# Performance work log

Hardware: AMD Instinct MI355X
Metric: run time of the kernel (lower is better)

The kernel has to match this reference:

```python
import jax, jax.numpy as jnp
import numpy as np

B = 64      # num graphs
NPG = 800   # nodes per graph
N = B * NPG
EPG = 6400  # edges per graph (avg degree 8)
APG = 64    # feasible actions per graph
H = 4       # attention heads
C = 64      # hidden channels per head
OUT = 128   # out_channels


def _gat_params(key, fin, h, c, concat):
    k1, k2, k3 = jax.random.split(key, 3)
    s = 1.0 / np.sqrt(fin)
    W = jax.random.uniform(k1, (fin, h * c), jnp.float32, -s, s)
    a_src = jax.random.uniform(k2, (h, c), jnp.float32, -s, s)
    a_dst = jax.random.uniform(k3, (h, c), jnp.float32, -s, s)
    b = jnp.zeros((h * c if concat else c,), jnp.float32)
    return W, a_src, a_dst, b


def _lin_params(key, fin, fout):
    k1, k2 = jax.random.split(key)
    s = 1.0 / np.sqrt(fin)
    W = jax.random.uniform(k1, (fin, fout), jnp.float32, -s, s)
    b = jax.random.uniform(k2, (fout,), jnp.float32, -s, s)
    return W, b


def setup_inputs() -> dict:
    key = jax.random.key(0)
    ks = list(jax.random.split(key, 24))
    x = jax.random.normal(ks[0], (N, 5), jnp.float32)
    offs = jnp.arange(B, dtype=jnp.int32) * NPG
    src = jax.random.randint(ks[1], (B, EPG), 0, NPG, jnp.int32) + offs[:, None]
    dst = jax.random.randint(ks[2], (B, EPG), 0, NPG, jnp.int32) + offs[:, None]
    edge_index = jnp.stack([src.reshape(-1), dst.reshape(-1)])
    batch = jnp.repeat(jnp.arange(B, dtype=jnp.int32), NPG)
    actions_idx = (jax.random.randint(ks[3], (B, APG, 2), 0, NPG, jnp.int32)
                   + offs[:, None, None]).reshape(-1, 2)
    tabu_label = (jax.random.uniform(ks[4], (B * APG, 1)) < 0.5).astype(jnp.float32)
    inp = dict(x=x, edge_index=edge_index, batch=batch,
               actions_idx=actions_idx, tabu_label=tabu_label)
    names = ['f1', 'f2', 'f3', 'b1', 'b2', 'b3']
    fins = [3, H * C, H * C, 3, H * C, H * C]
    hs = [H, H, 1, H, H, 1]
    cs = [C, C, OUT, C, C, OUT]
    concats = [True, True, False, True, True, False]
    for i, nm in enumerate(names):
        W, a_s, a_d, b = _gat_params(ks[5 + i], fins[i], hs[i], cs[i], concats[i])
        inp[nm + '_W'] = W; inp[nm + '_as'] = a_s; inp[nm + '_ad'] = a_d; inp[nm + '_b'] = b
    dims = [(8 * OUT + 1, 2 * OUT), (2 * OUT, 2 * OUT), (2 * OUT, 2 * OUT), (2 * OUT, 1)]
    for i, (fi, fo) in enumerate(dims):
        W, b = _lin_params(ks[12 + i], fi, fo)
        inp['p_W%d' % (i + 1)] = W; inp['p_b%d' % (i + 1)] = b
    return inp


def _gat(h, s, d, W, a_src, a_dst, bias, concat):
    # PyG GATConv: project, per-edge attention, softmax over target index, scatter-add
    n = h.shape[0]
    Hh, Cc = a_src.shape
    xp = (h @ W).reshape(n, Hh, Cc)                      # [N,H,C]
    al_s = (xp * a_src).sum(-1)                          # [N,H]
    al_d = (xp * a_dst).sum(-1)                          # [N,H]
    e = jax.nn.leaky_relu(al_s[s] + al_d[d], 0.2)        # [E,H]
    m = jax.ops.segment_max(e, d, num_segments=n)
    ex = jnp.exp(e - m[d])
    den = jax.ops.segment_sum(ex, d, num_segments=n)
    alpha = ex / (den[d] + 1e-16)
    out = jax.ops.segment_sum(xp[s] * alpha[..., None], d, num_segments=n)  # [N,H,C]
    out = out.reshape(n, Hh * Cc) if concat else out.mean(axis=1)
    return out + bias


def reference(x, edge_index, batch, actions_idx, tabu_label,
              f1_W, f1_as, f1_ad, f1_b, f2_W, f2_as, f2_ad, f2_b,
              f3_W, f3_as, f3_ad, f3_b, b1_W, b1_as, b1_ad, b1_b,
              b2_W, b2_as, b2_ad, b2_b, b3_W, b3_as, b3_ad, b3_b,
              p_W1, p_b1, p_W2, p_b2, p_W3, p_b3, p_W4, p_b4):
    n = x.shape[0]
    ar = jnp.arange(n, dtype=edge_index.dtype)
    ei = jnp.concatenate([edge_index, jnp.stack([ar, ar])], axis=1)  # add_self_loops
    src, dst = ei[0], ei[1]
    # forward branch (flow source_to_target)
    hf = x[:, jnp.array([0, 1, 3])]
    hf = jax.nn.elu(_gat(hf, src, dst, f1_W, f1_as, f1_ad, f1_b, True))
    hf = jax.nn.elu(_gat(hf, src, dst, f2_W, f2_as, f2_ad, f2_b, True))
    hf3 = _gat(hf, src, dst, f3_W, f3_as, f3_ad, f3_b, False)
    # backward branch (flow target_to_source == reversed edges)
    hb = x[:, jnp.array([0, 2, 4])]
    hb = jax.nn.elu(_gat(hb, dst, src, b1_W, b1_as, b1_ad, b1_b, True))
    hb = jax.nn.elu(_gat(hb, dst, src, b2_W, b2_as, b2_ad, b2_b, True))
    hb3 = _gat(hb, dst, src, b3_W, b3_as, b3_ad, b3_b, False)
    h_node = jnp.concatenate([hf3, hb3], axis=-1)        # [N, 2*OUT]
    counts = jax.ops.segment_sum(jnp.ones((n,), x.dtype), batch, num_segments=B)
    g_pool = jax.ops.segment_sum(h_node, batch, num_segments=B) / counts[:, None]
    node_h = jnp.concatenate([h_node, g_pool[batch]], axis=-1)  # [N, 4*OUT]
    action_h = jnp.concatenate([node_h[actions_idx[:, 0]],
                                node_h[actions_idx[:, 1]],
                                tabu_label], axis=-1)    # [A, 8*OUT+1]
    h = jnp.tanh(action_h @ p_W1 + p_b1)
    h = jnp.tanh(h @ p_W2 + p_b2)
    h = jnp.tanh(h @ p_W3 + p_b3)
    score = (h @ p_W4 + p_b4).reshape(B, APG)
    log_prob = jax.nn.log_softmax(score, axis=-1)        # [B, APG]
    entropy = -(jnp.exp(log_prob) * log_prob).sum(-1, keepdims=True)  # [B,1]
    return (log_prob, entropy)
```

## Files before the change

kernel.cpp:

```cpp
#include <hip/hip_runtime.h>
#include <hip/hip_bf16.h>
#include <math.h>

constexpr int NN  = 51200;
constexpr int EE  = 409600;
constexpr int BB  = 64;
constexpr int APG = 64;
constexpr int NPG = 800;
constexpr int SCAN_N = 2 * NN;
constexpr int NA = BB * APG;
constexpr int KF = 1056;

typedef __bf16 bf16x8 __attribute__((ext_vector_type(8)));
typedef float f32x4 __attribute__((ext_vector_type(4)));
typedef float f32x2 __attribute__((ext_vector_type(2)));
typedef __attribute__((address_space(1))) const void g_void;
typedef __attribute__((address_space(3))) void l_void;

__device__ __forceinline__ float leaky(float x) { return x > 0.f ? x : 0.2f * x; }
__device__ __forceinline__ float bflo(unsigned w) { return __uint_as_float(w << 16); }
__device__ __forceinline__ float bfhi(unsigned w) { return __uint_as_float(w & 0xffff0000u); }
__device__ __forceinline__ unsigned short f2b(float x) {
  __hip_bfloat16 h = __float2bfloat16(x);
  unsigned short u;
  __builtin_memcpy(&u, &h, 2);
  return u;
}
__device__ __forceinline__ unsigned pack2(float a, float b) {
  return (unsigned)f2b(a) | ((unsigned)f2b(b) << 16);
}

__global__ void count_kernel(const int* __restrict__ ei, int* cnt) {
  int e = blockIdx.x * blockDim.x + threadIdx.x;
  if (e >= EE) return;
  int s = ei[e], d = ei[EE + e];
  atomicAdd(&cnt[d], 1);
  atomicAdd(&cnt[NN + s], 1);
}

__global__ __launch_bounds__(256) void scan1_kernel(const int* __restrict__ cnt,
                                                    int* __restrict__ rp,
                                                    int* __restrict__ bsum) {
  __shared__ int wsum[4];
  int b = blockIdx.x, t = threadIdx.x;
  int base = b * 1024 + t * 4;
  int4 v = *(const int4*)(cnt + base);
  int s = v.x + v.y + v.z + v.w;
  int lane = t & 63, wv = t >> 6;
  int incl = s;
  for (int off = 1; off < 64; off <<= 1) {
    int u = __shfl_up(incl, off);
    if (lane >= off) incl += u;
  }
  if (lane == 63) wsum[wv] = incl;
  __syncthreads();
  int woff = 0;
  for (int i = 0; i < wv; i++) woff += wsum[i];
  int excl = woff + incl - s;
  rp[base] = excl;
  rp[base + 1] = excl + v.x;
  rp[base + 2] = excl + v.x + v.y;
  rp[base + 3] = excl + v.x + v.y + v.z;
  if (t == 255) bsum[b] = woff + incl;
}

__global__ void scan2_kernel(const int* __restrict__ bsum, int* __restrict__ boff,
                             int* __restrict__ rp) {
  __shared__ int w0;
  int t = threadIdx.x;
  int v = (t < 100) ? bsum[t] : 0;
  int lane = t & 63;
  int incl = v;
  for (int off = 1; off < 64; off <<= 1) {
    int u = __shfl_up(incl, off);
    if (lane >= off) incl += u;
  }
  if (t == 63) w0 = incl;
  __syncthreads();
  int excl = incl - v + ((t >= 64) ? w0 : 0);
  if (t < 100) boff[t] = excl;
  if (t == 99) rp[SCAN_N] = excl + v;
}

__global__ __launch_bounds__(256) void scan3_kernel(int* __restrict__ rp,
                                                    const int* __restrict__ boff) {
  int b = blockIdx.x;
  int off = boff[b];
  int i = b * 1024 + threadIdx.x * 4;
  int4 v = *(int4*)(rp + i);
  v.x += off; v.y += off; v.z += off; v.w += off;
  *(int4*)(rp + i) = v;
}

__global__ void fill_kernel(const int* __restrict__ ei, const int* __restrict__ rp,
                            int* pos, int* __restrict__ col) {
  int e = blockIdx.x * blockDim.x + threadIdx.x;
  if (e >= EE) return;
  int s = ei[e], d = ei[EE + e];
  int p = atomicAdd(&pos[d], 1);
  col[rp[d] + p] = s;
  int q = atomicAdd(&pos[NN + s], 1);
  col[rp[NN + s] + q] = d;
}

__global__ __launch_bounds__(256) void precomp_kernel(const float* __restrict__ Wf,
                                                      const float* __restrict__ Wb,
                                                      const float* __restrict__ asf,
                                                      const float* __restrict__ adf,
                                                      const float* __restrict__ asb,
                                                      const float* __restrict__ adb,
                                                      float* __restrict__ wa) {
  int wave = (blockIdx.x * blockDim.x + threadIdx.x) >> 6;
  int lane = threadIdx.x & 63;
  if (wave >= 48) return;
  int dir = wave / 24, sd = (wave / 12) % 2, h = (wave / 3) % 4, c = wave % 3;
  const float* W = dir ? Wb : Wf;
  const float* a = dir ? (sd ? adb : asb) : (sd ? adf : asf);
  float v = W[c * 256 + h * 64 + lane] * a[h * 64 + lane];
  for (int off = 1; off < 64; off <<= 1) v += __shfl_xor(v, off);
  if (lane == 0) wa[wave] = v;
}

__global__ __launch_bounds__(256) void lin1_kernel(const float* __restrict__ x,
                                                   const float* __restrict__ Wf,
                                                   const float* __restrict__ Wb,
                                                   __hip_bfloat16* __restrict__ out) {
  int idx = blockIdx.x * 256 + threadIdx.x;
  int n = idx >> 5, grp = idx & 31;
  int dir = (n >= NN) ? 1 : 0;
  int node = dir ? n - NN : n;
  const float* W = dir ? Wb : Wf;
  int c1 = dir ? 2 : 1, c2 = dir ? 4 : 3;
  float f0 = x[node * 5], f1 = x[node * 5 + c1], f2 = x[node * 5 + c2];
  int j0 = grp * 8;
  float v[8];
#pragma unroll
  for (int j = 0; j < 8; j++)
    v[j] = f0 * W[j0 + j] + f1 * W[256 + j0 + j] + f2 * W[512 + j0 + j];
  uint4 u;
  u.x = pack2(v[0], v[1]);
  u.y = pack2(v[2], v[3]);
  u.z = pack2(v[4], v[5]);
  u.w = pack2(v[6], v[7]);
  *(uint4*)(out + (size_t)n * 256 + j0) = u;
}

__global__ __launch_bounds__(256) void al1_kernel(const float* __restrict__ x,
                                                  const float* __restrict__ wa,
                                                  float* __restrict__ al_s,
                                                  float* __restrict__ al_d) {
  int idx = blockIdx.x * 256 + threadIdx.x;
  int n = idx >> 2, h = idx & 3;
  int dir = (n >= NN) ? 1 : 0;
  int node = dir ? n - NN : n;
  int c1 = dir ? 2 : 1, c2 = dir ? 4 : 3;
  float f0 = x[node * 5], f1 = x[node * 5 + c1], f2 = x[node * 5 + c2];
  const float* ws = wa + dir * 24 + h * 3;
  const float* wd = wa + dir * 24 + 12 + h * 3;
  al_s[idx] = f0 * ws[0] + f1 * ws[1] + f2 * ws[2];
  al_d[idx] = f0 * wd[0] + f1 * wd[1] + f2 * wd[2];
}

template <int HH>
__global__ __launch_bounds__(256) void alpha_kernel(const float* __restrict__ als,
                                                    const float* __restrict__ ald,
                                                    const int* __restrict__ rp,
                                                    const int* __restrict__ col,
                                                    float* __restrict__ alpha,
                                                    float* __restrict__ alpha_self) {
  int b = blockIdx.x;
  int xcd = b & 7, q = b >> 3;
  int g2 = (q / 25) * 8 + xcd;
  int d = g2 * 800 + (q % 25) * 32 + (threadIdx.x >> 3);
  int slot = threadIdx.x & 7;
  int off_row = (d >= NN) ? NN : 0;
  float ald_loc[HH], self_lg[HH];
#pragma unroll
  for (int h = 0; h < HH; h++) {
    ald_loc[h] = ald[d * HH + h];
    self_lg[h] = leaky(als[d * HH + h] + ald_loc[h]);
  }
  int beg = rp[d], end = rp[d + 1];
  int i0 = beg + slot;
  bool have = i0 < end;
  int s0 = col[have ? i0 : beg] + off_row;
  float mx[HH], lg0[HH];
#pragma unroll
  for (int h = 0; h < HH; h++) mx[h] = self_lg[h];
  if (have) {
#pragma unroll
    for (int h = 0; h < HH; h++) {
      lg0[h] = leaky(als[s0 * HH + h] + ald_loc[h]);
      mx[h] = fmaxf(mx[h], lg0[h]);
    }
  }
  for (int i = i0 + 8; i < end; i += 8) {
    int s = col[i] + off_row;
#pragma unroll
    for (int h = 0; h < HH; h++) mx[h] = fmaxf(mx[h], leaky(als[s * HH + h] + ald_loc[h]));
  }
#pragma unroll
  for (int h = 0; h < HH; h++) {
    mx[h] = fmaxf(mx[h], __shfl_xor(mx[h], 1));
    mx[h] = fmaxf(mx[h], __shfl_xor(mx[h], 2));
    mx[h] = fmaxf(mx[h], __shfl_xor(mx[h], 4));
  }
  float sm[HH], w0[HH];
#pragma unroll
  for (int h = 0; h < HH; h++) sm[h] = 0.f;
  if (have) {
#pragma unroll
    for (int h = 0; h < HH; h++) {
      w0[h] = __expf(lg0[h] - mx[h]);
      sm[h] += w0[h];
    }
  }
  for (int i = i0 + 8; i < end; i += 8) {
    int s = col[i] + off_row;
#pragma unroll
    for (int h = 0; h < HH; h++) {
      float w = __expf(leaky(als[s * HH + h] + ald_loc[h]) - mx[h]);
      sm[h] += w;
      alpha[(size_t)i * HH + h] = w;
    }
  }
#pragma unroll
  for (int h = 0; h < HH; h++) {
    sm[h] += __shfl_xor(sm[h], 1);
    sm[h] += __shfl_xor(sm[h], 2);
    sm[h] += __shfl_xor(sm[h], 4);
  }
  float inv[HH];
#pragma unroll
  for (int h = 0; h < HH; h++)
    inv[h] = 1.f / (sm[h] + __expf(self_lg[h] - mx[h]) + 1e-16f);
  if (have) {
#pragma unroll
    for (int h = 0; h < HH; h++) alpha[(size_t)i0 * HH + h] = w0[h] * inv[h];
  }
  for (int i = i0 + 8; i < end; i += 8)
#pragma unroll
    for (int h = 0; h < HH; h++) alpha[(size_t)i * HH + h] *= inv[h];
  if (slot == 0) {
#pragma unroll
    for (int h = 0; h < HH; h++)
      alpha_self[d * HH + h] = __expf(self_lg[h] - mx[h]) * inv[h];
  }
}

template <int ND>
__device__ __forceinline__ void load_dw(const unsigned* p, unsigned* w) {
  if constexpr (ND == 4) {
    uint4 v = *(const uint4*)p;
    w[0] = v.x; w[1] = v.y; w[2] = v.z; w[3] = v.w;
  } else {
    uint2 v = *(const uint2*)p;
    w[0] = v.x; w[1] = v.y;
  }
}
__device__ __forceinline__ f32x2 unpk(unsigned w) {
  f32x2 v;
  v.x = bflo(w);
  v.y = bfhi(w);
  return v;
}

template <int HH, int CC, int OUT_SPLIT>
__global__ __launch_bounds__(256) void spmm_kernel(const __hip_bfloat16* __restrict__ xp,
                                                   const float* __restrict__ alpha,
                                                   const float* __restrict__ alpha_self,
                                                   const int* __restrict__ rp,
                                                   const int* __restrict__ col,
                                                   const float* __restrict__ biasf,
                                                   const float* __restrict__ biasb,
                                                   __hip_bfloat16* __restrict__ out_bf,
                                                   int do_elu) {
  constexpr int HC = HH * CC;
  constexpr int CPL = HC / 32;
  constexpr int NW = CPL / 2;
  int b = blockIdx.x;
  int xcd = b & 7, q = b >> 3;
  int g2 = (q / 200) * 8 + xcd;
  int d = g2 * 800 + (q % 200) * 4 + (threadIdx.x >> 6);
  int off_row = (d >= NN) ? NN : 0;
  const float* bias = (d >= NN) ? biasb : biasf;
  int lane = threadIdx.x & 63;
  int sub = lane & 31, g = lane >> 5;
  int h_l = (sub * CPL) / CC;
  const unsigned* xw = (const unsigned*)xp;
  size_t rowoff = (size_t)sub * NW;
  f32x2 acc[NW];
#pragma unroll
  for (int j = 0; j < NW; j++) acc[j] = (f32x2)(0.f);
  int beg = rp[d], end = rp[d + 1];
  int deg = end - beg;
  if (g == 0) {
    float a = alpha_self[d * HH + h_l];
    unsigned w[NW];
    load_dw<NW>(xw + (size_t)d * (HC / 2) + rowoff, w);
#pragma unroll
    for (int q2 = 0; q2 < NW; q2++) acc[q2] += a * unpk(w[q2]);
  }
  for (int it = 0; it * 4 < deg; it++) {
    int e1 = beg + it * 4 + g;
    int e2 = e1 + 2;
    bool p1 = e1 < end, p2 = e2 < end;
    int ec1 = p1 ? e1 : beg, ec2 = p2 ? e2 : beg;
    int s1 = col[ec1] + off_row, s2 = col[ec2] + off_row;
    float a1 = p1 ? alpha[(size_t)ec1 * HH + h_l] : 0.f;
    float a2 = p2 ? alpha[(size_t)ec2 * HH + h_l] : 0.f;
    unsigned w1[NW], w2[NW];
    load_dw<NW>(xw + (size_t)s1 * (HC / 2) + rowoff, w1);
    load_dw<NW>(xw + (size_t)s2 * (HC / 2) + rowoff, w2);
#pragma unroll
    for (int q2 = 0; q2 < NW; q2++)
      acc[q2] += a1 * unpk(w1[q2]) + a2 * unpk(w2[q2]);
  }
#pragma unroll
  for (int j = 0; j < NW; j++) {
    acc[j].x += __shfl_xor(acc[j].x, 32);
    acc[j].y += __shfl_xor(acc[j].y, 32);
  }
  if (g == 0) {
    float v[CPL];
#pragma unroll
    for (int j = 0; j < NW; j++) {
      v[2 * j] = acc[j].x + bias[sub * CPL + 2 * j];
      v[2 * j + 1] = acc[j].y + bias[sub * CPL + 2 * j + 1];
    }
    if (do_elu) {
#pragma unroll
      for (int j = 0; j < CPL; j++) v[j] = v[j] > 0.f ? v[j] : (__expf(v[j]) - 1.f);
    }
    unsigned* ob;
    if constexpr (OUT_SPLIT) {
      int nd = (d < NN) ? d : d - NN;
      int oo = (d < NN) ? 0 : 64;
      ob = (unsigned*)out_bf + (size_t)nd * 128 + oo + sub * NW;
    } else {
      ob = (unsigned*)out_bf + (size_t)d * (HC / 2) + rowoff;
    }
#pragma unroll
    for (int q2 = 0; q2 < NW; q2++)
      ob[q2] = pack2(v[2 * q2], v[2 * q2 + 1]);
  }
}

__global__ void castW2_kernel(const float* __restrict__ W0, const float* __restrict__ W1,
                              __hip_bfloat16* __restrict__ Wt0,
                              __hip_bfloat16* __restrict__ Wt1,
                              int K, int N, int Kp) {
  int idx = blockIdx.x * 256 + threadIdx.x;
  int tot = N * Kp;
  if (idx >= 2 * tot) return;
  const float* W = (idx < tot) ? W0 : W1;
  __hip_bfloat16* Wt = (idx < tot) ? Wt0 : Wt1;
  int i = (idx < tot) ? idx : idx - tot;
  int n = i / Kp, k = i % Kp;
  Wt[i] = (k < K) ? __float2bfloat16(W[(size_t)k * N + n]) : __float2bfloat16(0.f);
}

template <int EPI, int ALH, int ALCC>
__global__ __launch_bounds__(256) void gemm_mfma(const __hip_bfloat16* __restrict__ A,
                                                 const __hip_bfloat16* __restrict__ Bt0,
                                                 const __hip_bfloat16* __restrict__ Bt1,
                                                 __hip_bfloat16* __restrict__ Cb,
                                                 const float* __restrict__ bias0,
                                                 const float* __restrict__ bias1,
                                                 const float* __restrict__ asv0,
                                                 const float* __restrict__ asv1,
                                                 const float* __restrict__ adv0,
                                                 const float* __restrict__ adv1,
                                                 float* __restrict__ al_s,
                                                 float* __restrict__ al_d,
                                                 int M, int N, int K, int Mhalf) {
  __shared__ __align__(16) __hip_bfloat16 As[128 * 32];
  __shared__ __align__(16) __hip_bfloat16 Bs[128 * 32];
  int t = threadIdx.x;
  int wave = t >> 6, lane = t & 63;
  int wm = (wave >> 1) * 64, wn = (wave & 1) * 64;
  int bm = blockIdx.y * 128, bn = blockIdx.x * 128;
  bool second = bm >= Mhalf;
  const __hip_bfloat16* Bt = second ? Bt1 : Bt0;
  const float* bias = second ? bias1 : bias0;
  const float* asv = second ? asv1 : asv0;
  const float* adv = second ? adv1 : adv0;

  int r0 = t >> 2, c0 = (t & 3) * 8;
  const __hip_bfloat16* Ag0 = A + (size_t)(bm + r0) * K + c0;
  const __hip_bfloat16* Ag1 = A + (size_t)(bm + r0 + 64) * K + c0;
  const __hip_bfloat16* Bg0 = Bt + (size_t)(bn + r0) * K + c0;
  const __hip_bfloat16* Bg1 = Bt + (size_t)(bn + r0 + 64) * K + c0;
  __hip_bfloat16* Asp0 = As + t * 8;
  __hip_bfloat16* Asp1 = As + 64 * 8 * 4 + t * 8;
  __hip_bfloat16* Bsp0 = Bs + t * 8;
  __hip_bfloat16* Bsp1 = Bs + 64 * 8 * 4 + t * 8;

  f32x4 acc[4][4];
#pragma unroll
  for (int i = 0; i < 4; i++)
#pragma unroll
    for (int j = 0; j < 4; j++) acc[i][j] = (f32x4)(0.f);

  int frag_off = (lane & 15) * 32 + (lane >> 4) * 8;
  const __hip_bfloat16* Ab = As + wm * 32 + frag_off;
  const __hip_bfloat16* Bb = Bs + wn * 32 + frag_off;

  for (int k0 = 0; k0 < K; k0 += 32) {
    __syncthreads();
    __builtin_amdgcn_global_load_lds((g_void*)(Ag0 + k0), (l_void*)Asp0, 16, 0, 0);
    __builtin_amdgcn_global_load_lds((g_void*)(Ag1 + k0), (l_void*)Asp1, 16, 0, 0);
    __builtin_amdgcn_global_load_lds((g_void*)(Bg0 + k0), (l_void*)Bsp0, 16, 0, 0);
    __builtin_amdgcn_global_load_lds((g_void*)(Bg1 + k0), (l_void*)Bsp1, 16, 0, 0);
    __syncthreads();
    bf16x8 af[4], bfr[4];
#pragma unroll
    for (int i = 0; i < 4; i++) af[i] = *(const bf16x8*)(Ab + i * 16 * 32);
#pragma unroll
    for (int j = 0; j < 4; j++) bfr[j] = *(const bf16x8*)(Bb + j * 16 * 32);
#pragma unroll
    for (int i = 0; i < 4; i++)
#pragma unroll
      for (int j = 0; j < 4; j++)
        acc[i][j] = __builtin_amdgcn_mfma_f32_16x16x32_bf16(af[i], bfr[j], acc[i][j], 0, 0, 0);
  }

  int cr = (lane >> 4) * 4, cc = lane & 15;

  if constexpr (ALH > 0) {
    int head = (bn + wn) / ALCC;
    float as_c[4], ad_c[4];
#pragma unroll
    for (int j = 0; j < 4; j++) {
      int colx = bn + wn + j * 16 + cc;
      as_c[j] = asv[colx];
      ad_c[j] = adv[colx];
    }
#pragma unroll
    for (int i = 0; i < 4; i++)
#pragma unroll
      for (int r = 0; r < 4; r++) {
        float ps = 0.f, pd = 0.f;
#pragma unroll
        for (int j = 0; j < 4; j++) {
          ps += acc[i][j][r] * as_c[j];
          pd += acc[i][j][r] * ad_c[j];
        }
        ps += __shfl_xor(ps, 1); pd += __shfl_xor(pd, 1);
        ps += __shfl_xor(ps, 2); pd += __shfl_xor(pd, 2);
        ps += __shfl_xor(ps, 4); pd += __shfl_xor(pd, 4);
        ps += __shfl_xor(ps, 8); pd += __shfl_xor(pd, 8);
        if ((lane & 15) == 0) {
          int row = bm + wm + i * 16 + cr + r;
          if (ALCC > 64) {
            atomicAdd(&al_s[row * ALH + head], ps);
            atomicAdd(&al_d[row * ALH + head], pd);
          } else {
            al_s[row * ALH + head] = ps;
            al_d[row * ALH + head] = pd;
          }
        }
      }
  }

#pragma unroll
  for (int i = 0; i < 4; i++)
#pragma unroll
    for (int j = 0; j < 4; j++) {
      int colx = bn + wn + j * 16 + cc;
      float bs = (EPI == 2) ? bias[colx] : 0.f;
#pragma unroll
      for (int r = 0; r < 4; r++) {
        float v = acc[i][j][r];
        if (EPI == 2) v = tanhf(v + bs);
        Cb[(size_t)(bm + wm + i * 16 + cr + r) * N + colx] = __float2bfloat16(v);
      }
    }
}

__global__ void pool1_kernel(const __hip_bfloat16* __restrict__ h_node,
                             float* __restrict__ part) {
  int g = blockIdx.y, c = blockIdx.x, t = threadIdx.x;
  const unsigned* base = (const unsigned*)h_node + ((size_t)g * NPG + c * 100) * 128 + t;
  f32x2 s = (f32x2)(0.f);
  for (int i = 0; i < 100; i++) {
    unsigned w = base[(size_t)i * 128];
    s += unpk(w);
  }
  part[(size_t)(g * 8 + c) * 256 + 2 * t] = s.x;
  part[(size_t)(g * 8 + c) * 256 + 2 * t + 1] = s.y;
}

__global__ void pool2_kernel(const float* __restrict__ part, float* __restrict__ g_pool) {
  int g = blockIdx.x, t = threadIdx.x;
  float s = 0.f;
  for (int c = 0; c < 8; c++) s += part[(size_t)(g * 8 + c) * 256 + t];
  g_pool[g * 256 + t] = s * (1.f / NPG);
}

__global__ __launch_bounds__(256) void buildfeat_kernel(const __hip_bfloat16* __restrict__ h_node,
                                                        const float* __restrict__ g_pool,
                                                        const int* __restrict__ actions,
                                                        const float* __restrict__ tabu,
                                                        const int* __restrict__ batch,
                                                        __hip_bfloat16* __restrict__ feat) {
  int a = (blockIdx.x * blockDim.x + threadIdx.x) >> 6;
  int lane = threadIdx.x & 63;
  if (a >= NA) return;
  int n0 = actions[a * 2], n1 = actions[a * 2 + 1];
  int g = batch[n0];
  ushort4 v0 = *(const ushort4*)(h_node + (size_t)n0 * 256 + lane * 4);
  float4 vg = *(const float4*)(g_pool + (size_t)g * 256 + lane * 4);
  ushort4 v1 = *(const ushort4*)(h_node + (size_t)n1 * 256 + lane * 4);
  __hip_bfloat16* fr = feat + (size_t)a * KF;
  ushort4 ug = make_ushort4(f2b(vg.x), f2b(vg.y), f2b(vg.z), f2b(vg.w));
  *(ushort4*)(fr + lane * 4) = v0;
  *(ushort4*)(fr + 256 + lane * 4) = ug;
  *(ushort4*)(fr + 512 + lane * 4) = v1;
  *(ushort4*)(fr + 768 + lane * 4) = ug;
  if (lane < 8) {
    float t0 = (lane == 0) ? tabu[a] : 0.f;
    ushort4 u = make_ushort4(f2b(t0), 0, 0, 0);
    *(ushort4*)(fr + 1024 + lane * 4) = u;
  }
}

__global__ __launch_bounds__(256) void gemv_kernel(const __hip_bfloat16* __restrict__ y,
                                                   const float* __restrict__ W4,
                                                   const float* __restrict__ b4,
                                                   float* __restrict__ scores) {
  int a = (blockIdx.x * blockDim.x + threadIdx.x) >> 6;
  int lane = threadIdx.x & 63;
  if (a >= NA) return;
  const unsigned* row = (const unsigned*)(y + (size_t)a * 256);
  float s = 0.f;
#pragma unroll
  for (int q = 0; q < 2; q++) {
    unsigned w = row[lane * 2 + q];
    s += bflo(w) * W4[lane * 4 + 2 * q] + bfhi(w) * W4[lane * 4 + 2 * q + 1];
  }
  for (int off = 1; off < 64; off <<= 1) s += __shfl_xor(s, off);
  if (lane == 0) scores[a] = s + b4[0];
}

__global__ void softmax_kernel(const float* __restrict__ scores, float* __restrict__ out) {
  int g = (blockIdx.x * blockDim.x + threadIdx.x) >> 6;
  int lane = threadIdx.x & 63;
  if (g >= BB) return;
  float s = scores[g * 64 + lane];
  float m = s;
  for (int off = 1; off < 64; off <<= 1) m = fmaxf(m, __shfl_xor(m, off));
  float ex = expf(s - m);
  float sum = ex;
  for (int off = 1; off < 64; off <<= 1) sum += __shfl_xor(sum, off);
  float lp = s - m - logf(sum);
  out[g * 64 + lane] = lp;
  float pe = (ex / sum) * lp;
  for (int off = 1; off < 64; off <<= 1) pe += __shfl_xor(pe, off);
  if (lane == 0) out[BB * APG + g] = -pe;
}

extern "C" void kernel_launch(void* const* d_in, const int* in_sizes, int n_in,
                              void* d_out, int out_size, void* d_ws, size_t ws_size,
                              hipStream_t stream) {
  const float* x = (const float*)d_in[0];
  const int* ei = (const int*)d_in[1];
  const int* batch = (const int*)d_in[2];
  const int* actions = (const int*)d_in[3];
  const float* tabu = (const float*)d_in[4];
  const float* fW[3] = {(const float*)d_in[5], (const float*)d_in[9], (const float*)d_in[13]};
  const float* fas[3] = {(const float*)d_in[6], (const float*)d_in[10], (const float*)d_in[14]};
  const float* fad[3] = {(const float*)d_in[7], (const float*)d_in[11], (const float*)d_in[15]};
  const float* fb[3] = {(const float*)d_in[8], (const float*)d_in[12], (const float*)d_in[16]};
  const float* bW[3] = {(const float*)d_in[17], (const float*)d_in[21], (const float*)d_in[25]};
  const float* bas[3] = {(const float*)d_in[18], (const float*)d_in[22], (const float*)d_in[26]};
  const float* bad[3] = {(const float*)d_in[19], (const float*)d_in[23], (const float*)d_in[27]};
  const float* bb[3] = {(const float*)d_in[20], (const float*)d_in[24], (const float*)d_in[28]};
  const float* pW1 = (const float*)d_in[29];
  const float* pb1 = (const float*)d_in[30];
  const float* pW2 = (const float*)d_in[31];
  const float* pb2 = (const float*)d_in[32];
  const float* pW3 = (const float*)d_in[33];
  const float* pb3 = (const float*)d_in[34];
  const float* pW4 = (const float*)d_in[35];
  const float* pb4 = (const float*)d_in[36];
  float* out = (float*)d_out;

  char* ws = (char*)d_ws;
  size_t o = 0;
  auto alloc = [&](size_t bytes) -> void* {
    o = (o + 255) & ~(size_t)255;
    void* p = ws + o;
    o += bytes;
    return p;
  };
  int* cnt = (int*)alloc((size_t)4 * NN * 4);
  int* rp = (int*)alloc((size_t)(SCAN_N + 1) * 4);
  int* col = (int*)alloc(((size_t)2 * EE + 64) * 4);
  int* bsum = (int*)alloc(128 * 4);
  int* boff = (int*)alloc(128 * 4);
  float* al_s = (float*)alloc((size_t)SCAN_N * 4 * 4);
  float* al_d = (float*)alloc((size_t)SCAN_N * 4 * 4);
  float* alpha = (float*)alloc((size_t)2 * EE * 4 * 4);
  float* alpha_self = (float*)alloc((size_t)SCAN_N * 4 * 4);
  float* wa = (float*)alloc(64 * 4);
  __hip_bfloat16* xp = (__hip_bfloat16*)alloc((size_t)SCAN_N * 256 * 2);
  __hip_bfloat16* bufA = (__hip_bfloat16*)alloc((size_t)SCAN_N * 256 * 2);
  __hip_bfloat16* h_node = (__hip_bfloat16*)alloc((size_t)NN * 256 * 2);
  __hip_bfloat16* wt0 = (__hip_bfloat16*)alloc((size_t)256 * KF * 2);
  __hip_bfloat16* wt1 = (__hip_bfloat16*)alloc((size_t)256 * KF * 2);
  float* part = (float*)alloc((size_t)BB * 8 * 256 * 4);
  float* g_pool = (float*)alloc((size_t)BB * 256 * 4);
  float* scores = (float*)alloc((size_t)NA * 4);
  __hip_bfloat16* feat = xp;
  __hip_bfloat16* y1 = feat + (size_t)NA * KF;
  __hip_bfloat16* y2 = y1 + (size_t)NA * 256;

  hipMemsetAsync(cnt, 0, (size_t)4 * NN * 4, stream);
  count_kernel<<<(EE + 255) / 256, 256, 0, stream>>>(ei, cnt);
  scan1_kernel<<<SCAN_N / 1024, 256, 0, stream>>>(cnt, rp, bsum);
  scan2_kernel<<<1, 128, 0, stream>>>(bsum, boff, rp);
  scan3_kernel<<<SCAN_N / 1024, 256, 0, stream>>>(rp, boff);
  fill_kernel<<<(EE + 255) / 256, 256, 0, stream>>>(ei, rp, cnt + 2 * NN, col);

  const int nwb = SCAN_N / 4;
  const int nab = SCAN_N * 8 / 256;

  precomp_kernel<<<12, 256, 0, stream>>>(fW[0], bW[0], fas[0], fad[0], bas[0], bad[0], wa);
  lin1_kernel<<<SCAN_N * 32 / 256, 256, 0, stream>>>(x, fW[0], bW[0], xp);
  al1_kernel<<<SCAN_N * 4 / 256, 256, 0, stream>>>(x, wa, al_s, al_d);
  alpha_kernel<4><<<nab, 256, 0, stream>>>(al_s, al_d, rp, col, alpha, alpha_self);
  spmm_kernel<4, 64, 0><<<nwb, 256, 0, stream>>>(xp, alpha, alpha_self, rp, col,
                                                 fb[0], bb[0], bufA, 1);
  castW2_kernel<<<(2 * 256 * 256 + 255) / 256, 256, 0, stream>>>(fW[1], bW[1], wt0, wt1,
                                                                 256, 256, 256);
  gemm_mfma<1, 4, 64><<<dim3(2, SCAN_N / 128), 256, 0, stream>>>(
      bufA, wt0, wt1, xp, nullptr, nullptr, fas[1], bas[1], fad[1], bad[1],
      al_s, al_d, SCAN_N, 256, 256, NN);
  alpha_kernel<4><<<nab, 256, 0, stream>>>(al_s, al_d, rp, col, alpha, alpha_self);
  spmm_kernel<4, 64, 0><<<nwb, 256, 0, stream>>>(xp, alpha, alpha_self, rp, col,
                                                 fb[1], bb[1], bufA, 1);
  castW2_kernel<<<(2 * 128 * 256 + 255) / 256, 256, 0, stream>>>(fW[2], bW[2], wt0, wt1,
                                                                 256, 128, 256);
  hipMemsetAsync(al_s, 0, (size_t)SCAN_N * 4, stream);
  hipMemsetAsync(al_d, 0, (size_t)SCAN_N * 4, stream);
  gemm_mfma<1, 1, 128><<<dim3(1, SCAN_N / 128), 256, 0, stream>>>(
      bufA, wt0, wt1, xp, nullptr, nullptr, fas[2], bas[2], fad[2], bad[2],
      al_s, al_d, SCAN_N, 128, 256, NN);
  alpha_kernel<1><<<nab, 256, 0, stream>>>(al_s, al_d, rp, col, alpha, alpha_self);
  spmm_kernel<1, 128, 1><<<nwb, 256, 0, stream>>>(xp, alpha, alpha_self, rp, col,
                                                  fb[2], bb[2], h_node, 0);

  pool1_kernel<<<dim3(8, BB), 128, 0, stream>>>(h_node, part);
  pool2_kernel<<<BB, 256, 0, stream>>>(part, g_pool);

  buildfeat_kernel<<<NA / 4, 256, 0, stream>>>(h_node, g_pool, actions, tabu, batch, feat);
  castW2_kernel<<<(2 * 256 * KF + 255) / 256, 256, 0, stream>>>(pW1, pW1, wt0, wt1,
                                                                1025, 256, KF);
  gemm_mfma<2, 0, 64><<<dim3(2, NA / 128), 256, 0, stream>>>(
      feat, wt0, wt0, y1, pb1, pb1, nullptr, nullptr, nullptr, nullptr,
      nullptr, nullptr, NA, 256, KF, 1 << 30);
  castW2_kernel<<<(2 * 256 * 256 + 255) / 256, 256, 0, stream>>>(pW2, pW3, wt0, wt1,
                                                                 256, 256, 256);
  gemm_mfma<2, 0, 64><<<dim3(2, NA / 128), 256, 0, stream>>>(
      y1, wt0, wt0, y2, pb2, pb2, nullptr, nullptr, nullptr, nullptr,
      nullptr, nullptr, NA, 256, 256, 1 << 30);
  gemm_mfma<2, 0, 64><<<dim3(2, NA / 128), 256, 0, stream>>>(
      y2, wt1, wt1, y1, pb3, pb3, nullptr, nullptr, nullptr, nullptr,
      nullptr, nullptr, NA, 256, 256, 1 << 30);
  gemv_kernel<<<NA / 4, 256, 0, stream>>>(y1, pW4, pb4, scores);
  softmax_kernel<<<(BB * 64) / 256, 256, 0, stream>>>(scores, out);
}
```

Baseline: 536.4 us.

## Switch intermediates to fp16 with packed half2 SpMM accumulation; fuse gemv and softmax

All intermediate feature buffers, weights and MFMA GEMMs move from bf16 to fp16. The SpMM aggregation now accumulates in packed half2 FMAs instead of unpacking to fp32, which cuts the VALU work per gathered edge. The final gemv and log-softmax/entropy kernels are merged into one per-graph head kernel, removing a launch and the scores round trip. Accumulating in fp16 risks precision loss and overflow on large neighbourhood sums.

Result: slower. 548.4 us (+2.2%).

```diff
diff --git a/kernel.cpp b/kernel.cpp
--- a/kernel.cpp
+++ b/kernel.cpp
@@ -1,5 +1,5 @@
 #include <hip/hip_runtime.h>
-#include <hip/hip_bf16.h>
+#include <hip/hip_fp16.h>
 #include <math.h>
 
 constexpr int NN  = 51200;
@@ -11,23 +11,35 @@
 constexpr int NA = BB * APG;
 constexpr int KF = 1056;
 
-typedef __bf16 bf16x8 __attribute__((ext_vector_type(8)));
+typedef _Float16 f16x8 __attribute__((ext_vector_type(8)));
 typedef float f32x4 __attribute__((ext_vector_type(4)));
 typedef float f32x2 __attribute__((ext_vector_type(2)));
 typedef __attribute__((address_space(1))) const void g_void;
 typedef __attribute__((address_space(3))) void l_void;
 
 __device__ __forceinline__ float leaky(float x) { return x > 0.f ? x : 0.2f * x; }
-__device__ __forceinline__ float bflo(unsigned w) { return __uint_as_float(w << 16); }
-__device__ __forceinline__ float bfhi(unsigned w) { return __uint_as_float(w & 0xffff0000u); }
-__device__ __forceinline__ unsigned short f2b(float x) {
-  __hip_bfloat16 h = __float2bfloat16(x);
-  unsigned short u;
-  __builtin_memcpy(&u, &h, 2);
+__device__ __forceinline__ unsigned pack2h(float a, float b) {
+  __half2 h = __floats2half2_rn(a, b);
+  unsigned u;
+  __builtin_memcpy(&u, &h, 4);
   return u;
 }
-__device__ __forceinline__ unsigned pack2(float a, float b) {
-  return (unsigned)f2b(a) | ((unsigned)f2b(b) << 16);
+__device__ __forceinline__ __half2 bit2h(unsigned w) {
+  __half2 h;
+  __builtin_memcpy(&h, &w, 4);
+  return h;
+}
+__device__ __forceinline__ unsigned h2bit(__half2 h) {
+  unsigned u;
+  __builtin_memcpy(&u, &h, 4);
+  return u;
+}
+__device__ __forceinline__ f32x2 unpk_h(unsigned w) {
+  float2 f = __half22float2(bit2h(w));
+  f32x2 r;
+  r.x = f.x;
+  r.y = f.y;
+  return r;
 }
 
 __global__ void count_kernel(const int* __restrict__ ei, int* cnt) {
@@ -124,7 +136,7 @@
 __global__ __launch_bounds__(256) void lin1_kernel(const float* __restrict__ x,
                                                    const float* __restrict__ Wf,
                                                    const float* __restrict__ Wb,
-                                                   __hip_bfloat16* __restrict__ out) {
+                                                   __half* __restrict__ out) {
   int idx = blockIdx.x * 256 + threadIdx.x;
   int n = idx >> 5, grp = idx & 31;
   int dir = (n >= NN) ? 1 : 0;
@@ -138,10 +150,10 @@
   for (int j = 0; j < 8; j++)
     v[j] = f0 * W[j0 + j] + f1 * W[256 + j0 + j] + f2 * W[512 + j0 + j];
   uint4 u;
-  u.x = pack2(v[0], v[1]);
-  u.y = pack2(v[2], v[3]);
-  u.z = pack2(v[4], v[5]);
-  u.w = pack2(v[6], v[7]);
+  u.x = pack2h(v[0], v[1]);
+  u.y = pack2h(v[2], v[3]);
+  u.z = pack2h(v[4], v[5]);
+  u.w = pack2h(v[6], v[7]);
   *(uint4*)(out + (size_t)n * 256 + j0) = u;
 }
 
@@ -258,22 +270,16 @@
     w[0] = v.x; w[1] = v.y;
   }
 }
-__device__ __forceinline__ f32x2 unpk(unsigned w) {
-  f32x2 v;
-  v.x = bflo(w);
-  v.y = bfhi(w);
-  return v;
-}
 
 template <int HH, int CC, int OUT_SPLIT>
-__global__ __launch_bounds__(256) void spmm_kernel(const __hip_bfloat16* __restrict__ xp,
+__global__ __launch_bounds__(256) void spmm_kernel(const __half* __restrict__ xp,
                                                    const float* __restrict__ alpha,
                                                    const float* __restrict__ alpha_self,
                                                    const int* __restrict__ rp,
                                                    const int* __restrict__ col,
                                                    const float* __restrict__ biasf,
                                                    const float* __restrict__ biasb,
-                                                   __hip_bfloat16* __restrict__ out_bf,
+                                                   __half* __restrict__ out_h,
                                                    int do_elu) {
   constexpr int HC = HH * CC;
   constexpr int CPL = HC / 32;
@@ -289,17 +295,17 @@
   int h_l = (sub * CPL) / CC;
   const unsigned* xw = (const unsigned*)xp;
   size_t rowoff = (size_t)sub * NW;
-  f32x2 acc[NW];
-#pragma unroll
-  for (int j = 0; j < NW; j++) acc[j] = (f32x2)(0.f);
+  __half2 acc[NW];
+#pragma unroll
+  for (int j = 0; j < NW; j++) acc[j] = __floats2half2_rn(0.f, 0.f);
   int beg = rp[d], end = rp[d + 1];
   int deg = end - beg;
   if (g == 0) {
-    float a = alpha_self[d * HH + h_l];
+    __half2 a = __float2half2_rn(alpha_self[d * HH + h_l]);
     unsigned w[NW];
     load_dw<NW>(xw + (size_t)d * (HC / 2) + rowoff, w);
 #pragma unroll
-    for (int q2 = 0; q2 < NW; q2++) acc[q2] += a * unpk(w[q2]);
+    for (int q2 = 0; q2 < NW; q2++) acc[q2] = __hfma2(a, bit2h(w[q2]), acc[q2]);
   }
   for (int it = 0; it * 4 < deg; it++) {
     int e1 = beg + it * 4 + g;
@@ -307,26 +313,29 @@
     bool p1 = e1 < end, p2 = e2 < end;
     int ec1 = p1 ? e1 : beg, ec2 = p2 ? e2 : beg;
     int s1 = col[ec1] + off_row, s2 = col[ec2] + off_row;
-    float a1 = p1 ? alpha[(size_t)ec1 * HH + h_l] : 0.f;
-    float a2 = p2 ? alpha[(size_t)ec2 * HH + h_l] : 0.f;
+    __half2 a1 = __float2half2_rn(p1 ? alpha[(size_t)ec1 * HH + h_l] : 0.f);
+    __half2 a2 = __float2half2_rn(p2 ? alpha[(size_t)ec2 * HH + h_l] : 0.f);
     unsigned w1[NW], w2[NW];
     load_dw<NW>(xw + (size_t)s1 * (HC / 2) + rowoff, w1);
     load_dw<NW>(xw + (size_t)s2 * (HC / 2) + rowoff, w2);
 #pragma unroll
-    for (int q2 = 0; q2 < NW; q2++)
-      acc[q2] += a1 * unpk(w1[q2]) + a2 * unpk(w2[q2]);
+    for (int q2 = 0; q2 < NW; q2++) {
+      acc[q2] = __hfma2(a1, bit2h(w1[q2]), acc[q2]);
+      acc[q2] = __hfma2(a2, bit2h(w2[q2]), acc[q2]);
+    }
   }
 #pragma unroll
   for (int j = 0; j < NW; j++) {
-    acc[j].x += __shfl_xor(acc[j].x, 32);
-    acc[j].y += __shfl_xor(acc[j].y, 32);
+    unsigned u = __shfl_xor(h2bit(acc[j]), 32);
+    acc[j] = __hadd2(acc[j], bit2h(u));
   }
   if (g == 0) {
     float v[CPL];
 #pragma unroll
     for (int j = 0; j < NW; j++) {
-      v[2 * j] = acc[j].x + bias[sub * CPL + 2 * j];
-      v[2 * j + 1] = acc[j].y + bias[sub * CPL + 2 * j + 1];
+      float2 f = __half22float2(acc[j]);
+      v[2 * j] = f.x + bias[sub * CPL + 2 * j];
+      v[2 * j + 1] = f.y + bias[sub * CPL + 2 * j + 1];
     }
     if (do_elu) {
 #pragma unroll
@@ -336,35 +345,34 @@
     if constexpr (OUT_SPLIT) {
       int nd = (d < NN) ? d : d - NN;
       int oo = (d < NN) ? 0 : 64;
-      ob = (unsigned*)out_bf + (size_t)nd * 128 + oo + sub * NW;
+      ob = (unsigned*)out_h + (size_t)nd * 128 + oo + sub * NW;
     } else {
-      ob = (unsigned*)out_bf + (size_t)d * (HC / 2) + rowoff;
+      ob = (unsigned*)out_h + (size_t)d * (HC / 2) + rowoff;
     }
 #pragma unroll
     for (int q2 = 0; q2 < NW; q2++)
-      ob[q2] = pack2(v[2 * q2], v[2 * q2 + 1]);
+      ob[q2] = pack2h(v[2 * q2], v[2 * q2 + 1]);
   }
 }
 
 __global__ void castW2_kernel(const float* __restrict__ W0, const float* __restrict__ W1,
-                              __hip_bfloat16* __restrict__ Wt0,
-                              __hip_bfloat16* __restrict__ Wt1,
+                              __half* __restrict__ Wt0, __half* __restrict__ Wt1,
                               int K, int N, int Kp) {
   int idx = blockIdx.x * 256 + threadIdx.x;
   int tot = N * Kp;
   if (idx >= 2 * tot) return;
   const float* W = (idx < tot) ? W0 : W1;
-  __hip_bfloat16* Wt = (idx < tot) ? Wt0 : Wt1;
+  __half* Wt = (idx < tot) ? Wt0 : Wt1;
   int i = (idx < tot) ? idx : idx - tot;
   int n = i / Kp, k = i % Kp;
-  Wt[i] = (k < K) ? __float2bfloat16(W[(size_t)k * N + n]) : __float2bfloat16(0.f);
+  Wt[i] = (k < K) ? __float2half(W[(size_t)k * N + n]) : __float2half(0.f);
 }
 
 template <int EPI, int ALH, int ALCC>
-__global__ __launch_bounds__(256) void gemm_mfma(const __hip_bfloat16* __restrict__ A,
-                                                 const __hip_bfloat16* __restrict__ Bt0,
-                                                 const __hip_bfloat16* __restrict__ Bt1,
-                                                 __hip_bfloat16* __restrict__ Cb,
+__global__ __launch_bounds__(256) void gemm_mfma(const __half* __restrict__ A,
+                                                 const __half* __restrict__ Bt0,
+                                                 const __half* __restrict__ Bt1,
+                                                 __half* __restrict__ Cb,
                                                  const float* __restrict__ bias0,
                                                  const float* __restrict__ bias1,
                                                  const float* __restrict__ asv0,
@@ -374,27 +382,27 @@
                                                  float* __restrict__ al_s,
                                                  float* __restrict__ al_d,
                                                  int M, int N, int K, int Mhalf) {
-  __shared__ __align__(16) __hip_bfloat16 As[128 * 32];
-  __shared__ __align__(16) __hip_bfloat16 Bs[128 * 32];
+  __shared__ __align__(16) __half As[128 * 32];
+  __shared__ __align__(16) __half Bs[128 * 32];
   int t = threadIdx.x;
   int wave = t >> 6, lane = t & 63;
   int wm = (wave >> 1) * 64, wn = (wave & 1) * 64;
   int bm = blockIdx.y * 128, bn = blockIdx.x * 128;
   bool second = bm >= Mhalf;
-  const __hip_bfloat16* Bt = second ? Bt1 : Bt0;
+  const __half* Bt = second ? Bt1 : Bt0;
   const float* bias = second ? bias1 : bias0;
   const float* asv = second ? asv1 : asv0;
   const float* adv = second ? adv1 : adv0;
 
   int r0 = t >> 2, c0 = (t & 3) * 8;
-  const __hip_bfloat16* Ag0 = A + (size_t)(bm + r0) * K + c0;
-  const __hip_bfloat16* Ag1 = A + (size_t)(bm + r0 + 64) * K + c0;
-  const __hip_bfloat16* Bg0 = Bt + (size_t)(bn + r0) * K + c0;
-  const __hip_bfloat16* Bg1 = Bt + (size_t)(bn + r0 + 64) * K + c0;
-  __hip_bfloat16* Asp0 = As + t * 8;
-  __hip_bfloat16* Asp1 = As + 64 * 8 * 4 + t * 8;
-  __hip_bfloat16* Bsp0 = Bs + t * 8;
-  __hip_bfloat16* Bsp1 = Bs + 64 * 8 * 4 + t * 8;
+  const __half* Ag0 = A + (size_t)(bm + r0) * K + c0;
+  const __half* Ag1 = A + (size_t)(bm + r0 + 64) * K + c0;
+  const __half* Bg0 = Bt + (size_t)(bn + r0) * K + c0;
+  const __half* Bg1 = Bt + (size_t)(bn + r0 + 64) * K + c0;
+  __half* Asp0 = As + t * 8;
+  __half* Asp1 = As + 64 * 8 * 4 + t * 8;
+  __half* Bsp0 = Bs + t * 8;
+  __half* Bsp1 = Bs + 64 * 8 * 4 + t * 8;
 
   f32x4 acc[4][4];
 #pragma unroll
@@ -403,8 +411,8 @@
     for (int j = 0; j < 4; j++) acc[i][j] = (f32x4)(0.f);
 
   int frag_off = (lane & 15) * 32 + (lane >> 4) * 8;
-  const __hip_bfloat16* Ab = As + wm * 32 + frag_off;
-  const __hip_bfloat16* Bb = Bs + wn * 32 + frag_off;
+  const __half* Ab = As + wm * 32 + frag_off;
+  const __half* Bb = Bs + wn * 32 + frag_off;
 
   for (int k0 = 0; k0 < K; k0 += 32) {
     __syncthreads();
@@ -413,16 +421,16 @@
     __builtin_amdgcn_global_load_lds((g_void*)(Bg0 + k0), (l_void*)Bsp0, 16, 0, 0);
     __builtin_amdgcn_global_load_lds((g_void*)(Bg1 + k0), (l_void*)Bsp1, 16, 0, 0);
     __syncthreads();
-    bf16x8 af[4], bfr[4];
-#pragma unroll
-    for (int i = 0; i < 4; i++) af[i] = *(const bf16x8*)(Ab + i * 16 * 32);
-#pragma unroll
-    for (int j = 0; j < 4; j++) bfr[j] = *(const bf16x8*)(Bb + j * 16 * 32);
+    f16x8 af[4], bfr[4];
+#pragma unroll
+    for (int i = 0; i < 4; i++) af[i] = *(const f16x8*)(Ab + i * 16 * 32);
+#pragma unroll
+    for (int j = 0; j < 4; j++) bfr[j] = *(const f16x8*)(Bb + j * 16 * 32);
 #pragma unroll
     for (int i = 0; i < 4; i++)
 #pragma unroll
       for (int j = 0; j < 4; j++)
-        acc[i][j] = __builtin_amdgcn_mfma_f32_16x16x32_bf16(af[i], bfr[j], acc[i][j], 0, 0, 0);
+        acc[i][j] = __builtin_amdgcn_mfma_f32_16x16x32_f16(af[i], bfr[j], acc[i][j], 0, 0, 0);
   }
 
   int cr = (lane >> 4) * 4, cc = lane & 15;
@@ -473,20 +481,17 @@
       for (int r = 0; r < 4; r++) {
         float v = acc[i][j][r];
         if (EPI == 2) v = tanhf(v + bs);
-        Cb[(size_t)(bm + wm + i * 16 + cr + r) * N + colx] = __float2bfloat16(v);
+        Cb[(size_t)(bm + wm + i * 16 + cr + r) * N + colx] = __float2half(v);
       }
     }
 }
 
-__global__ void pool1_kernel(const __hip_bfloat16* __restrict__ h_node,
+__global__ void pool1_kernel(const __half* __restrict__ h_node,
                              float* __restrict__ part) {
   int g = blockIdx.y, c = blockIdx.x, t = threadIdx.x;
   const unsigned* base = (const unsigned*)h_node + ((size_t)g * NPG + c * 100) * 128 + t;
   f32x2 s = (f32x2)(0.f);
-  for (int i = 0; i < 100; i++) {
-    unsigned w = base[(size_t)i * 128];
-    s += unpk(w);
-  }
+  for (int i = 0; i < 100; i++) s += unpk_h(base[(size_t)i * 128]);
   part[(size_t)(g * 8 + c) * 256 + 2 * t] = s.x;
   part[(size_t)(g * 8 + c) * 256 + 2 * t + 1] = s.y;
 }
@@ -498,12 +503,12 @@
   g_pool[g * 256 + t] = s * (1.f / NPG);
 }
 
-__global__ __launch_bounds__(256) void buildfeat_kernel(const __hip_bfloat16* __restrict__ h_node,
+__global__ __launch_bounds__(256) void buildfeat_kernel(const __half* __restrict__ h_node,
                                                         const float* __restrict__ g_pool,
                                                         const int* __restrict__ actions,
                                                         const float* __restrict__ tabu,
                                                         const int* __restrict__ batch,
-                                                        __hip_bfloat16* __restrict__ feat) {
+                                                        __half* __restrict__ feat) {
   int a = (blockIdx.x * blockDim.x + threadIdx.x) >> 6;
   int lane = threadIdx.x & 63;
   if (a >= NA) return;
@@ -512,52 +517,57 @@
   ushort4 v0 = *(const ushort4*)(h_node + (size_t)n0 * 256 + lane * 4);
   float4 vg = *(const float4*)(g_pool + (size_t)g * 256 + lane * 4);
   ushort4 v1 = *(const ushort4*)(h_node + (size_t)n1 * 256 + lane * 4);
-  __hip_bfloat16* fr = feat + (size_t)a * KF;
-  ushort4 ug = make_ushort4(f2b(vg.x), f2b(vg.y), f2b(vg.z), f2b(vg.w));
+  __half* fr = feat + (size_t)a * KF;
+  uint2 ug;
+  ug.x = pack2h(vg.x, vg.y);
+  ug.y = pack2h(vg.z, vg.w);
   *(ushort4*)(fr + lane * 4) = v0;
-  *(ushort4*)(fr + 256 + lane * 4) = ug;
+  *(uint2*)(fr + 256 + lane * 4) = ug;
   *(ushort4*)(fr + 512 + lane * 4) = v1;
-  *(ushort4*)(fr + 768 + lane * 4) = ug;
+  *(uint2*)(fr + 768 + lane * 4) = ug;
   if (lane < 8) {
     float t0 = (lane == 0) ? tabu[a] : 0.f;
-    ushort4 u = make_ushort4(f2b(t0), 0, 0, 0);
-    *(ushort4*)(fr + 1024 + lane * 4) = u;
-  }
-}
-
-__global__ __launch_bounds__(256) void gemv_kernel(const __hip_bfloat16* __restrict__ y,
+    uint2 u;
+    u.x = pack2h(t0, 0.f);
+    u.y = 0;
+    *(uint2*)(fr + 1024 + lane * 4) = u;
+  }
+}
+
+__global__ __launch_bounds__(256) void head_kernel(const __half* __restrict__ y,
                                                    const float* __restrict__ W4,
                                                    const float* __restrict__ b4,
-                                                   float* __restrict__ scores) {
-  int a = (blockIdx.x * blockDim.x + threadIdx.x) >> 6;
-  int lane = threadIdx.x & 63;
-  if (a >= NA) return;
-  const unsigned* row = (const unsigned*)(y + (size_t)a * 256);
+                                                   float* __restrict__ out) {
+  __shared__ float sc[64];
+  int g = blockIdx.x;
+  int t = threadIdx.x;
+  int a = t >> 2, sub = t & 3;
+  int aid = g * 64 + a;
+  const unsigned* row = (const unsigned*)(y + (size_t)aid * 256) + sub * 32;
+  const float* w = W4 + sub * 64;
   float s = 0.f;
 #pragma unroll
-  for (int q = 0; q < 2; q++) {
-    unsigned w = row[lane * 2 + q];
-    s += bflo(w) * W4[lane * 4 + 2 * q] + bfhi(w) * W4[lane * 4 + 2 * q + 1];
-  }
-  for (int off = 1; off < 64; off <<= 1) s += __shfl_xor(s, off);
-  if (lane == 0) scores[a] = s + b4[0];
-}
-
-__global__ void softmax_kernel(const float* __restrict__ scores, float* __restrict__ out) {
-  int g = (blockIdx.x * blockDim.x + threadIdx.x) >> 6;
-  int lane = threadIdx.x & 63;
-  if (g >= BB) return;
-  float s = scores[g * 64 + lane];
-  float m = s;
-  for (int off = 1; off < 64; off <<= 1) m = fmaxf(m, __shfl_xor(m, off));
-  float ex = expf(s - m);
-  float sum = ex;
-  for (int off = 1; off < 64; off <<= 1) sum += __shfl_xor(sum, off);
-  float lp = s - m - logf(sum);
-  out[g * 64 + lane] = lp;
-  float pe = (ex / sum) * lp;
-  for (int off = 1; off < 64; off <<= 1) pe += __shfl_xor(pe, off);
-  if (lane == 0) out[BB * APG + g] = -pe;
+  for (int q = 0; q < 32; q++) {
+    f32x2 f = unpk_h(row[q]);
+    s += f.x * w[2 * q] + f.y * w[2 * q + 1];
+  }
+  s += __shfl_xor(s, 1);
+  s += __shfl_xor(s, 2);
+  if (sub == 0) sc[a] = s + b4[0];
+  __syncthreads();
+  if (t < 64) {
+    float v = sc[t];
+    float m = v;
+    for (int off = 1; off < 64; off <<= 1) m = fmaxf(m, __shfl_xor(m, off));
+    float ex = expf(v - m);
+    float sum = ex;
+    for (int off = 1; off < 64; off <<= 1) sum += __shfl_xor(sum, off);
+    float lp = v - m - logf(sum);
+    out[g * 64 + t] = lp;
+    float pe = (ex / sum) * lp;
+    for (int off = 1; off < 64; off <<= 1) pe += __shfl_xor(pe, off);
+    if (t == 0) out[BB * APG + g] = -pe;
+  }
 }
 
 extern "C" void kernel_launch(void* const* d_in, const int* in_sizes, int n_in,
@@ -604,17 +614,16 @@
   float* alpha = (float*)alloc((size_t)2 * EE * 4 * 4);
   float* alpha_self = (float*)alloc((size_t)SCAN_N * 4 * 4);
   float* wa = (float*)alloc(64 * 4);
-  __hip_bfloat16* xp = (__hip_bfloat16*)alloc((size_t)SCAN_N * 256 * 2);
-  __hip_bfloat16* bufA = (__hip_bfloat16*)alloc((size_t)SCAN_N * 256 * 2);
-  __hip_bfloat16* h_node = (__hip_bfloat16*)alloc((size_t)NN * 256 * 2);
-  __hip_bfloat16* wt0 = (__hip_bfloat16*)alloc((size_t)256 * KF * 2);
-  __hip_bfloat16* wt1 = (__hip_bfloat16*)alloc((size_t)256 * KF * 2);
+  __half* xp = (__half*)alloc((size_t)SCAN_N * 256 * 2);
+  __half* bufA = (__half*)alloc((size_t)SCAN_N * 256 * 2);
+  __half* h_node = (__half*)alloc((size_t)NN * 256 * 2);
+  __half* wt0 = (__half*)alloc((size_t)256 * KF * 2);
+  __half* wt1 = (__half*)alloc((size_t)256 * KF * 2);
   float* part = (float*)alloc((size_t)BB * 8 * 256 * 4);
   float* g_pool = (float*)alloc((size_t)BB * 256 * 4);
-  float* scores = (float*)alloc((size_t)NA * 4);
-  __hip_bfloat16* feat = xp;
-  __hip_bfloat16* y1 = feat + (size_t)NA * KF;
-  __hip_bfloat16* y2 = y1 + (size_t)NA * 256;
+  __half* feat = xp;
+  __half* y1 = feat + (size_t)NA * KF;
+  __half* y2 = y1 + (size_t)NA * 256;
 
   hipMemsetAsync(cnt, 0, (size_t)4 * NN * 4, stream);
   count_kernel<<<(EE + 255) / 256, 256, 0, stream>>>(ei, cnt);
@@ -668,6 +677,5 @@
   gemm_mfma<2, 0, 64><<<dim3(2, NA / 128), 256, 0, stream>>>(
       y2, wt1, wt1, y1, pb3, pb3, nullptr, nullptr, nullptr, nullptr,
       nullptr, nullptr, NA, 256, 256, 1 << 30);
-  gemv_kernel<<<NA / 4, 256, 0, stream>>>(y1, pW4, pb4, scores);
-  softmax_kernel<<<(BB * 64) / 256, 256, 0, stream>>>(scores, out);
-}
+  head_kernel<<<BB, 256, 0, stream>>>(y1, pW4, pb4, out);
+}
```
